# Kernel tuning notes

Measured on AMD Instinct MI355X. Metric: run time of the kernel, lower is better.

The kernel has to match this reference:

```python
import jax, jax.numpy as jnp
import numpy as np

T, B, E, H = 2048, 2, 1024, 16
D = E // H

def setup_inputs() -> dict:
    key = jax.random.key(0)
    ks = jax.random.split(key, 5)
    s = 1.0 / np.sqrt(E)  # keep projection weights at sane scale
    return {
        "query": jax.random.normal(ks[0], (T, B, E), jnp.float32),
        "Wq": jax.random.normal(ks[1], (E, E), jnp.float32) * s,
        "bq": jnp.zeros((E,), jnp.float32),
        "Wk": jax.random.normal(ks[2], (E, E), jnp.float32) * s,
        "bk": jnp.zeros((E,), jnp.float32),
        "Wv": jax.random.normal(ks[3], (E, E), jnp.float32) * s,
        "bv": jnp.zeros((E,), jnp.float32),
        "Wo": jax.random.normal(ks[4], (E, E), jnp.float32) * s,
        "bo": jnp.zeros((E,), jnp.float32),
    }

def reference(query, Wq, bq, Wk, bk, Wv, bv, Wo, bo):
    # query: [T, B, E] (fairseq time-first). self-attention path.
    scaling = D ** -0.5
    q = (query @ Wq.T + bq) * scaling          # [T,B,E]
    k = query @ Wk.T + bk                      # [T,B,E]
    v = query @ Wv.T + bv                      # [T,B,E]
    # split heads: [T,B,H,D]
    q = q.reshape(T, B, H, D)
    k = k.reshape(T, B, H, D)
    v = v.reshape(T, B, H, D)
    # attention scores [B,H,T,S]
    scores = jnp.einsum("tbhd,sbhd->bhts", q, k)
    probs = jax.nn.softmax(scores, axis=-1)
    # weighted values -> [T,B,H,D]
    attn = jnp.einsum("bhts,sbhd->tbhd", probs, v).reshape(T, B, E)
    return attn @ Wo.T + bo                    # [T,B,E]
```

## Files before the change

kernel.cpp:

```cpp
#include <hip/hip_runtime.h>
#include <hip/hip_bf16.h>

#define T_DIM 2048

typedef __attribute__((ext_vector_type(8))) short short8_t;
typedef short8_t __attribute__((may_alias)) short8_a;
typedef __attribute__((ext_vector_type(4))) short short4_t;
typedef short4_t __attribute__((may_alias)) short4_a;
typedef __attribute__((ext_vector_type(4))) float f32x4;
typedef __attribute__((ext_vector_type(16))) float f32x16;
typedef __attribute__((ext_vector_type(4))) float float4_t;
typedef float4_t __attribute__((may_alias)) float4_a;
typedef __attribute__((ext_vector_type(4))) unsigned int u32x4;

__device__ __forceinline__ short f2bf(float f) {
    unsigned int u = __builtin_bit_cast(unsigned int, f);
    unsigned int r = (u + 0x7fffu + ((u >> 16) & 1u)) >> 16;
    return (short)r;
}

__device__ __forceinline__ void gl_lds16(const short* g, short* l) {
    __builtin_amdgcn_global_load_lds(
        (const __attribute__((address_space(1))) void*)g,
        (__attribute__((address_space(3))) void*)l, 16, 0, 0);
}

__global__ __launch_bounds__(256) void cvt_all(const float* __restrict__ query,
                                               const float* __restrict__ Wq,
                                               const float* __restrict__ Wk,
                                               const float* __restrict__ Wv,
                                               const float* __restrict__ Wo,
                                               short* __restrict__ out) {
    const int bx = blockIdx.x;
    const int i = bx * 2048 + threadIdx.x * 8;
    const float* s;
    if (bx < 2048) {
        s = query + i;
    } else {
        int j = i - 4194304;
        int wsel = j >> 20;
        const float* wp = wsel == 0 ? Wq : (wsel == 1 ? Wk : (wsel == 2 ? Wv : Wo));
        s = wp + (j & 1048575);
    }
    float4_a a = *(const float4_a*)s;
    float4_a b = *(const float4_a*)(s + 4);
    short8_a r;
    r[0] = f2bf(a[0]); r[1] = f2bf(a[1]); r[2] = f2bf(a[2]); r[3] = f2bf(a[3]);
    r[4] = f2bf(b[0]); r[5] = f2bf(b[1]); r[6] = f2bf(b[2]); r[7] = f2bf(b[3]);
    *(short8_a*)(out + i) = r;
}

template <int BM, int BN, int MODE>
__global__ __launch_bounds__(256) void gemm_lds(const short* __restrict__ A,
                                                const short* __restrict__ W,
                                                const float* __restrict__ b0,
                                                const float* __restrict__ b1,
                                                const float* __restrict__ b2,
                                                short* __restrict__ o0,
                                                short* __restrict__ o1,
                                                short* __restrict__ o2,
                                                float* __restrict__ of) {
    constexpr int FM = BM / 32;
    constexpr int FN = BN / 32;
    __shared__ short As[BM * 32];
    __shared__ short Bs[BN * 32];

    const int tid = threadIdx.x;
    const int l = tid & 63, w = tid >> 6;
    const int wm = w >> 1, wn = w & 1;

    const int nbx = gridDim.x;
    const int nb = nbx * gridDim.y;
    const int bid = blockIdx.x + nbx * blockIdx.y;
    const int swz = (bid & 7) * (nb >> 3) + (bid >> 3);
    const int bx = swz % nbx, by = swz / nbx;

    const int m0 = by * BM, n0 = bx * BN;
    const int l15 = l & 15, l4 = l >> 4;
    const int lr = l >> 2, lc = (l & 3) * 8;

    f32x4 acc[FM][FN];
#pragma unroll
    for (int i = 0; i < FM; i++)
#pragma unroll
        for (int j = 0; j < FN; j++) {
            f32x4 z = {0.f, 0.f, 0.f, 0.f};
            acc[i][j] = z;
        }

    const short* Ab = A + (m0 + lr) * 1024 + lc;
    const short* Wb = W + (n0 + lr) * 1024 + lc;

    for (int k0 = 0; k0 < 1024; k0 += 32) {
#pragma unroll
        for (int j = 0; j < BM / 64; j++) {
            int base = (j * 4 + w) * 16;
            gl_lds16(Ab + base * 1024 + k0, &As[base * 32]);
        }
#pragma unroll
        for (int j = 0; j < BN / 64; j++) {
            int base = (j * 4 + w) * 16;
            gl_lds16(Wb + base * 1024 + k0, &Bs[base * 32]);
        }
        __syncthreads();

        short8_t af[FM], bf[FN];
#pragma unroll
        for (int m = 0; m < FM; m++)
            af[m] = *(const short8_a*)&As[(wm * (BM / 2) + m * 16 + l15) * 32 + l4 * 8];
#pragma unroll
        for (int n = 0; n < FN; n++)
            bf[n] = *(const short8_a*)&Bs[(wn * (BN / 2) + n * 16 + l15) * 32 + l4 * 8];
#pragma unroll
        for (int m = 0; m < FM; m++)
#pragma unroll
            for (int n = 0; n < FN; n++)
                acc[m][n] = __builtin_amdgcn_mfma_f32_16x16x32_bf16(af[m], bf[n], acc[m][n], 0, 0, 0);
        __syncthreads();
    }

    if (MODE == 3) {
#pragma unroll
        for (int n = 0; n < FN; n++) {
            int col = n0 + wn * (BN / 2) + n * 16 + l15;
            float bv = b0[col];
#pragma unroll
            for (int m = 0; m < FM; m++)
#pragma unroll
                for (int i = 0; i < 4; i++) {
                    int row = m0 + wm * (BM / 2) + m * 16 + l4 * 4 + i;
                    of[row * 1024 + col] = acc[m][n][i] + bv;
                }
        }
    } else {
        const int proj = n0 >> 10;
        const float* bias = proj == 0 ? b0 : (proj == 1 ? b1 : b2);
        short* outp = proj == 0 ? o0 : (proj == 1 ? o1 : o2);
#pragma unroll
        for (int n = 0; n < FN; n++) {
            int cw = (n0 + wn * (BN / 2) + n * 16 + l15) & 1023;
            float bv = bias[cw];
            int h = cw >> 6, d = cw & 63;
#pragma unroll
            for (int m = 0; m < FM; m++)
#pragma unroll
                for (int i = 0; i < 4; i++) {
                    int row = m0 + wm * (BM / 2) + m * 16 + l4 * 4 + i;
                    float v = acc[m][n][i] + bv;
                    if (proj == 0) v *= 0.18033688011112042f;
                    int bb = row & 1, t = row >> 1;
                    int bh = bb * 16 + h;
                    if (proj == 0)
                        outp[(bh * 2048 + t) * 64 + d] = f2bf(v);
                    else if (proj == 1)
                        outp[bh * 131072 + (t >> 6) * 4096 + (d >> 3) * 512 + (t & 63) * 8 + (d & 7)] = f2bf(v);
                    else
                        outp[bh * 131072 + (t >> 6) * 4096 + ((t & 63) >> 3) * 512 + d * 8 + (t & 7)] = f2bf(v);
                }
        }
    }
}

__global__ __launch_bounds__(512, 4) void flash_attn(const short* __restrict__ Q,
                                                     const short* __restrict__ K,
                                                     const short* __restrict__ Vt,
                                                     short* __restrict__ O) {
    __shared__ short Ks[4][64 * 64];
    __shared__ short Vs[4][64 * 64];

    const int tid = threadIdx.x, l = tid & 63, w = tid >> 6;
    const int w4 = w >> 1, g = w & 1;
    const int l31 = l & 31, hi = l >> 5;

    const int bid = blockIdx.x + (blockIdx.y << 4);
    const int swz = (bid & 7) * 64 + (bid >> 3);
    const int qt = swz & 15, bh = swz >> 4;

    const int b = bh >> 4, hh = bh & 15;
    const int qrow = qt * 128 + w4 * 32 + l31;

    const short* Qp = Q + bh * (T_DIM * 64);
    const short* Kp = K + bh * 131072;
    const short* Vp = Vt + bh * 131072;

    short8_t qf[4];
#pragma unroll
    for (int c = 0; c < 4; c++)
        qf[c] = *(const short8_a*)&Qp[qrow * 64 + c * 16 + hi * 8];

    f32x16 oacc[2];
    f32x16 lacc;
#pragma unroll
    for (int i = 0; i < 16; i++) { oacc[0][i] = 0.f; oacc[1][i] = 0.f; lacc[i] = 0.f; }

    short8_t ones;
#pragma unroll
    for (int j = 0; j < 8; j++) ones[j] = (short)0x3F80;

    const int wq = w & 3;
    const int p0 = 2 * wq, p1 = 2 * wq + 1;
    const short* sgK0 = Kp + p0 * 512 + l * 8;
    const short* sgK1 = Kp + p1 * 512 + l * 8;
    const short* sgV0 = Vp + p0 * 512 + l * 8;
    const short* sgV1 = Vp + p1 * 512 + l * 8;

    auto stage = [&](int t) {
        const int buf = t & 3, off = t * 4096;
        if (w < 4) {
            gl_lds16(sgK0 + off, &Ks[buf][p0 * 512]);
            gl_lds16(sgK1 + off, &Ks[buf][p1 * 512]);
        } else {
            gl_lds16(sgV0 + off, &Vs[buf][p0 * 512]);
            gl_lds16(sgV1 + off, &Vs[buf][p1 * 512]);
        }
    };

    auto qkhalf = [&](f32x16& s, int t, int r) {
        const short* kc = &Ks[t & 3][0];
#pragma unroll
        for (int c = 0; c < 4; c++) {
            short8_t kf = *(const short8_a*)&kc[(2 * c + hi) * 512 + (r * 32 + l31) * 8];
            if (c == 0) {
                f32x16 z;
#pragma unroll
                for (int i = 0; i < 16; i++) z[i] = 0.f;
                s = __builtin_amdgcn_mfma_f32_32x32x16_bf16(kf, qf[0], z, 0, 0, 0);
            } else {
                s = __builtin_amdgcn_mfma_f32_32x32x16_bf16(kf, qf[c], s, 0, 0, 0);
            }
        }
    };

    auto expackhalf = [&](f32x16& s, short8_t* pf2) {
#pragma unroll
        for (int i = 0; i < 16; i++) s[i] = exp2f(s[i]);
        unsigned pk8[8];
#pragma unroll
        for (int u = 0; u < 8; u++) {
            unsigned t;
            asm("v_cvt_pk_bf16_f32 %0, %1, %2" : "=v"(t) : "v"(s[2 * u]), "v"(s[2 * u + 1]));
            pk8[u] = t;
        }
#pragma unroll
        for (int cc = 0; cc < 2; cc++) {
            unsigned A0 = pk8[4 * cc + 0], B0 = pk8[4 * cc + 2];
            unsigned A1 = pk8[4 * cc + 1], B1 = pk8[4 * cc + 3];
            asm("v_permlane32_swap_b32 %0, %1" : "+v"(A0), "+v"(B0));
            asm("v_permlane32_swap_b32 %0, %1" : "+v"(A1), "+v"(B1));
            u32x4 pu = {A0, A1, B0, B1};
            pf2[cc] = __builtin_bit_cast(short8_t, pu);
        }
    };

    auto pv = [&](const short8_t* pf, int t) {
        const short* vc = &Vs[t & 3][0];
#pragma unroll
        for (int r = 0; r < 2; r++)
#pragma unroll
            for (int cc = 0; cc < 2; cc++) {
                short8_t p = pf[r * 2 + cc];
                lacc = __builtin_amdgcn_mfma_f32_32x32x16_bf16(ones, p, lacc, 0, 0, 0);
#pragma unroll
                for (int dd = 0; dd < 2; dd++) {
                    short8_t vf = *(const short8_a*)&vc[(4 * r + 2 * cc + hi) * 512 +
                                                        (dd * 32 + l31) * 8];
                    oacc[dd] = __builtin_amdgcn_mfma_f32_32x32x16_bf16(vf, p, oacc[dd], 0, 0, 0);
                }
            }
    };

    stage(0);
    stage(1);

    f32x16 s;
    short8_t pf[4];

    for (int p = 0; p < 16; ++p) {
        __syncthreads();
        if (p < 15) { stage(2 * p + 2); stage(2 * p + 3); }
        const int t = 2 * p + g;
        __builtin_amdgcn_s_setprio(1);
        qkhalf(s, t, 0);
        __builtin_amdgcn_s_setprio(0);
        expackhalf(s, &pf[0]);
        __builtin_amdgcn_s_setprio(1);
        qkhalf(s, t, 1);
        __builtin_amdgcn_s_setprio(0);
        expackhalf(s, &pf[2]);
        __builtin_amdgcn_s_setprio(1);
        pv(pf, t);
        __builtin_amdgcn_s_setprio(0);
    }

    __syncthreads();
    float* xo = (float*)&Ks[0][0];
    float* xml = (float*)&Vs[0][0];
    if (g == 1) {
#pragma unroll
        for (int dd = 0; dd < 2; dd++)
#pragma unroll
            for (int g4 = 0; g4 < 4; g4++) {
                f32x4 v = {oacc[dd][4 * g4], oacc[dd][4 * g4 + 1],
                           oacc[dd][4 * g4 + 2], oacc[dd][4 * g4 + 3]};
                *(float4_a*)&xo[w4 * 2048 + (dd * 4 + g4) * 256 + l * 4] = v;
            }
        xml[w4 * 64 + l] = lacc[0];
    }
    __syncthreads();
    if (g == 0) {
        float rl = 1.0f / (lacc[0] + xml[w4 * 64 + l]);
#pragma unroll
        for (int dd = 0; dd < 2; dd++)
#pragma unroll
            for (int g4 = 0; g4 < 4; g4++) {
                f32x4 o1 = *(const float4_a*)&xo[w4 * 2048 + (dd * 4 + g4) * 256 + l * 4];
                short4_t o4;
#pragma unroll
                for (int i = 0; i < 4; i++)
                    o4[i] = f2bf((oacc[dd][4 * g4 + i] + o1[i]) * rl);
                *(short4_a*)&O[(qrow * 2 + b) * 1024 + hh * 64 + dd * 32 + g4 * 8 + hi * 4] = o4;
            }
    }
}

extern "C" void kernel_launch(void* const* d_in, const int* in_sizes, int n_in,
                              void* d_out, int out_size, void* d_ws, size_t ws_size,
                              hipStream_t stream) {
    const float* query = (const float*)d_in[0];
    const float* Wq = (const float*)d_in[1];
    const float* bq = (const float*)d_in[2];
    const float* Wk = (const float*)d_in[3];
    const float* bk = (const float*)d_in[4];
    const float* Wv = (const float*)d_in[5];
    const float* bv = (const float*)d_in[6];
    const float* Wo = (const float*)d_in[7];
    const float* bo = (const float*)d_in[8];

    short* Xbf = (short*)d_ws;
    short* Wqb = Xbf + 4194304;
    short* Wkb = Wqb + 1048576;
    short* Wvb = Wkb + 1048576;
    short* Wob = Wvb + 1048576;
    short* Qb = Wob + 1048576;
    short* Kb = Qb + 4194304;
    short* Vtb = Kb + 4194304;
    short* attnb = Xbf;

    cvt_all<<<4096, 256, 0, stream>>>(query, Wq, Wk, Wv, Wo, Xbf);

    gemm_lds<128, 128, 4><<<dim3(24, 32), 256, 0, stream>>>(Xbf, Wqb, bq, bk, bv,
                                                            Qb, Kb, Vtb, nullptr);

    flash_attn<<<dim3(16, 32), 512, 0, stream>>>(Qb, Kb, Vtb, attnb);

    gemm_lds<64, 128, 3><<<dim3(8, 64), 256, 0, stream>>>(attnb, Wob, bo, nullptr, nullptr,
                                                          nullptr, nullptr, nullptr, (float*)d_out);
}
```

Before: 119.8 us.

## Software-pipeline PV of previous tile with QK of current tile

Restructures the attention loop so each iteration issues both QK halves for the current tile and then the PV matmul for the previous tile, with exp/pack moved after. The aim is to hide softmax exponent and packing latency behind independent MFMA work. V buffers grow from four to six so the delayed PV still reads valid data. This adds LDS usage, which may reduce occupancy, and raises register pressure from double-buffered probability fragments.

```diff
diff --git a/kernel.cpp b/kernel.cpp
--- a/kernel.cpp
+++ b/kernel.cpp
@@ -166,7 +166,7 @@
                                                      const short* __restrict__ Vt,
                                                      short* __restrict__ O) {
     __shared__ short Ks[4][64 * 64];
-    __shared__ short Vs[4][64 * 64];
+    __shared__ short Vs[6][64 * 64];
 
     const int tid = threadIdx.x, l = tid & 63, w = tid >> 6;
     const int w4 = w >> 1, g = w & 1;
@@ -205,11 +205,13 @@
     const short* sgV1 = Vp + p1 * 512 + l * 8;
 
     auto stage = [&](int t) {
-        const int buf = t & 3, off = t * 4096;
+        const int off = t * 4096;
         if (w < 4) {
+            const int buf = t & 3;
             gl_lds16(sgK0 + off, &Ks[buf][p0 * 512]);
             gl_lds16(sgK1 + off, &Ks[buf][p1 * 512]);
         } else {
+            const int buf = t % 6;
             gl_lds16(sgV0 + off, &Vs[buf][p0 * 512]);
             gl_lds16(sgV1 + off, &Vs[buf][p1 * 512]);
         }
@@ -253,7 +255,7 @@
     };
 
     auto pv = [&](const short8_t* pf, int t) {
-        const short* vc = &Vs[t & 3][0];
+        const short* vc = &Vs[t % 6][0];
 #pragma unroll
         for (int r = 0; r < 2; r++)
 #pragma unroll
@@ -272,25 +274,27 @@
     stage(0);
     stage(1);
 
-    f32x16 s;
-    short8_t pf[4];
-
-    for (int p = 0; p < 16; ++p) {
+    short8_t pfA[4], pfB[4];
+
+    auto body = [&](int p, short8_t* pfIn, short8_t* pfOut) {
         __syncthreads();
         if (p < 15) { stage(2 * p + 2); stage(2 * p + 3); }
         const int t = 2 * p + g;
+        f32x16 sa, sb;
         __builtin_amdgcn_s_setprio(1);
-        qkhalf(s, t, 0);
+        qkhalf(sa, t, 0);
+        qkhalf(sb, t, 1);
+        if (p > 0) pv(pfIn, t - 2);
         __builtin_amdgcn_s_setprio(0);
-        expackhalf(s, &pf[0]);
-        __builtin_amdgcn_s_setprio(1);
-        qkhalf(s, t, 1);
-        __builtin_amdgcn_s_setprio(0);
-        expackhalf(s, &pf[2]);
-        __builtin_amdgcn_s_setprio(1);
-        pv(pf, t);
-        __builtin_amdgcn_s_setprio(0);
-    }
+        expackhalf(sa, &pfOut[0]);
+        expackhalf(sb, &pfOut[2]);
+    };
+
+    for (int p = 0; p < 16; p += 2) {
+        body(p, pfB, pfA);
+        body(p + 1, pfA, pfB);
+    }
+    pv(pfB, 30 + g);
 
     __syncthreads();
     float* xo = (float*)&Ks[0][0];
```

New measurement: 137.5 us. 1.15x slower.
